# Kernel optimization log

Measured on AMD Instinct MI355X. Metric: run time of the kernel, lower is better.

The kernel has to match this reference:

```python
import jax, jax.numpy as jnp
import numpy as np

B, C, H, W = 4, 256, 64, 64
C8 = C // 8


def setup_inputs() -> dict:
    key = jax.random.key(0)
    ks = jax.random.split(key, 8)
    s = 1.0 / np.sqrt(C)
    return {
        "x_ccd": jax.random.normal(ks[0], (B, C, H, W), jnp.float32),
        "x_dem": jax.random.normal(ks[1], (B, C, H, W), jnp.float32),
        "Wq": jax.random.normal(ks[2], (C8, C), jnp.float32) * s,
        "bq": jax.random.normal(ks[3], (C8,), jnp.float32) * 0.01,
        "Wk": jax.random.normal(ks[4], (C8, C), jnp.float32) * s,
        "bk": jax.random.normal(ks[5], (C8,), jnp.float32) * 0.01,
        "Wv": jax.random.normal(ks[6], (C, C), jnp.float32) * s,
        "bv": jax.random.normal(ks[7], (C,), jnp.float32) * 0.01,
        "gamma": jnp.zeros((1,), jnp.float32),
    }


def reference(x_ccd, x_dem, Wq, bq, Wk, bk, Wv, bv, gamma):
    b, c, h, w = x_ccd.shape
    n = h * w
    xc = x_ccd.reshape(b, c, n)  # [B,C,N]
    xd = x_dem.reshape(b, c, n)
    # 1x1 convs == per-pixel linear projections
    q = jnp.einsum("oc,bcn->bno", Wq, xc) + bq  # [B,N,C8]
    k = jnp.einsum("oc,bcn->bon", Wk, xd) + bk[None, :, None]  # [B,C8,N]
    energy = jnp.einsum("bno,bom->bnm", q, k)  # [B,N,N]
    attention = jax.nn.softmax(energy, axis=-1)
    v = jnp.einsum("oc,bcn->bon", Wv, xd) + bv[None, :, None]  # [B,C,N]
    out = jnp.einsum("bom,bnm->bon", v, attention)  # value @ attention^T
    out = out.reshape(b, c, h, w)
    return gamma * out + x_ccd
```

## Files before the change

kernel.cpp:

```cpp
#include <hip/hip_runtime.h>

typedef unsigned short u16;
typedef unsigned int u32;
typedef short v8s __attribute__((ext_vector_type(8)));
typedef float v16f __attribute__((ext_vector_type(16)));

#define MFMA(a, b, c) __builtin_amdgcn_mfma_f32_32x32x16_bf16(a, b, c, 0, 0, 0)
#define L2E 1.44269504088896f

union U8 { v8s s; uint4 u4; u32 u[4]; };

__device__ __forceinline__ u16 f2bf(float x) {
    u32 u = __float_as_uint(x);
    return (u16)((u + 0x7FFFu + ((u >> 16) & 1u)) >> 16);
}
__device__ __forceinline__ u32 pk2(float a, float b) {
    return (u32)f2bf(a) | ((u32)f2bf(b) << 16);
}
__device__ __forceinline__ u32 pkz(float e0, float e1) {
    return __builtin_amdgcn_perm(__float_as_uint(e1), __float_as_uint(e0), 0x07060302u);
}


__global__ __launch_bounds__(256) void prep_w_kernel(
    const float* __restrict__ Wq, const float* __restrict__ bq,
    const float* __restrict__ Wk, const float* __restrict__ bk,
    const float* __restrict__ Wv, const float* __restrict__ bv,
    u16* __restrict__ WfT, float* __restrict__ ball)
{
    int tid = blockIdx.x * 256 + threadIdx.x;
    if (tid < 81920) {
        int ch = tid >> 8, c = tid & 255;
        float w;
        if (ch < 32)      w = Wq[ch * 256 + c];
        else if (ch < 64) w = Wk[(ch - 32) * 256 + c] * L2E;
        else              w = Wv[(ch - 64) * 256 + c];
        int tile = (ch >> 5) * 16 + (c >> 4);
        int lane = ((c >> 3) & 1) * 32 + (ch & 31);
        WfT[tile * 512 + lane * 8 + (c & 7)] = f2bf(w);
    } else if (tid < 82240) {
        int i = tid - 81920;
        float bb;
        if (i < 32)      bb = bq[i];
        else if (i < 64) bb = bk[i - 32] * L2E;
        else             bb = bv[i - 64];
        ball[i] = bb;
    }
}

__global__ __launch_bounds__(256, 2) void proj_kernel(
    const float* __restrict__ xc, const float* __restrict__ xd,
    const u16* __restrict__ WfT, const float* __restrict__ ball,
    u16* __restrict__ qfT, u16* __restrict__ kfT, u16* __restrict__ vfT)
{
    __shared__ u16 xls[2][32][264];
    int blk = blockIdx.x, b = blk >> 7, n0 = (blk & 127) * 32;
    int t = threadIdx.x, lane = t & 63, wv = t >> 6;
    int hl = lane >> 5, l31 = lane & 31;

#pragma unroll
    for (int p = 0; p < 4; p++) {
        int s = p * 256 + t;
        int arr = s >> 9, c4 = (s >> 3) & 63, n4s = s & 7;
        const float* src = arr ? xd : xc;
        size_t g0 = ((size_t)(b * 256 + c4 * 4)) * 4096 + n0 + n4s * 4;
        float4 r0 = *(const float4*)&src[g0];
        float4 r1 = *(const float4*)&src[g0 + 4096];
        float4 r2 = *(const float4*)&src[g0 + 8192];
        float4 r3 = *(const float4*)&src[g0 + 12288];
        *(uint2*)&xls[arr][n4s * 4 + 0][c4 * 4] = make_uint2(pk2(r0.x, r1.x), pk2(r2.x, r3.x));
        *(uint2*)&xls[arr][n4s * 4 + 1][c4 * 4] = make_uint2(pk2(r0.y, r1.y), pk2(r2.y, r3.y));
        *(uint2*)&xls[arr][n4s * 4 + 2][c4 * 4] = make_uint2(pk2(r0.z, r1.z), pk2(r2.z, r3.z));
        *(uint2*)&xls[arr][n4s * 4 + 3][c4 * 4] = make_uint2(pk2(r0.w, r1.w), pk2(r2.w, r3.w));
    }
    __syncthreads();

    int jobs[3];
    int nj;
    if (wv == 0)      { jobs[0] = 0; jobs[1] = 2; jobs[2] = 0; nj = 2; }
    else if (wv == 1) { jobs[0] = 1; jobs[1] = 3; jobs[2] = 0; nj = 2; }
    else if (wv == 2) { jobs[0] = 4; jobs[1] = 5; jobs[2] = 6; nj = 3; }
    else              { jobs[0] = 7; jobs[1] = 8; jobs[2] = 9; nj = 3; }

    int nt = blk & 127;
    int n = n0 + l31;
    int vl = ((n >> 3) & 1) * 32, tk = n >> 4, j8 = n & 7;

    for (int jj = 0; jj < nj; jj++) {
        int j = jobs[jj];
        int arr = (j != 0);
        const u16* wb = WfT + (size_t)(j * 16) * 512 + lane * 8;
        v16f acc = {};
#pragma unroll
        for (int kc = 0; kc < 16; kc++) {
            U8 bx, a;
            bx.u4 = *(const uint4*)&xls[arr][l31][kc * 16 + hl * 8];
            a.u4  = *(const uint4*)(wb + (size_t)kc * 512);
            acc = MFMA(a.s, bx.s, acc);
        }
        if (j <= 1) {
            u16* dst = j ? kfT : qfT;
#pragma unroll
            for (int i = 0; i < 8; i++) {
                int r = 2 * i;
                int row = (r & 3) + 8 * (r >> 2) + 4 * hl;
                float b0 = ball[j * 32 + row], b1 = ball[j * 32 + row + 1];
                u32 st = pk2(acc[r] + b0, acc[r + 1] + b1);
                size_t off = (((size_t)(b * 128 + nt) * 2 + (row >> 4)) * 512)
                           + (((row >> 3) & 1) * 32 + l31) * 8 + (row & 7);
                *(u32*)&dst[off] = st;
            }
        } else {
            int vi = j - 2;
            u16* vdst = vfT + (((size_t)(b * 8 + vi) * 256 + tk) * 512) + vl * 8 + j8;
#pragma unroll
            for (int r = 0; r < 16; r++) {
                int row = (r & 3) + 8 * (r >> 2) + 4 * hl;
                vdst[row * 8] = f2bf(acc[r] + ball[64 + vi * 32 + row]);
            }
        }
    }
}

__global__ __launch_bounds__(512, 2) void flash_kernel(
    const u16* __restrict__ qfT, const u16* __restrict__ kfT,
    const u16* __restrict__ vfT, const float* __restrict__ xccd,
    const float* __restrict__ gptr, float* __restrict__ outp)
{
    __shared__ float red[2][2][4][16][64];
    __shared__ float lred[2][32];

    const int t = threadIdx.x, lane = t & 63, wv = t >> 6;
    const int hl = lane >> 5, l31 = lane & 31;
    const int blk = blockIdx.x;
    const int b = (blk & 7) >> 1;
    const int qt = ((blk >> 3) << 1) | (blk & 1);
    const int kh = wv & 1, chh = (wv >> 1) & 1, qh = wv >> 2;
    const int n0 = qt * 64 + qh * 32;
    const int chbase = chh * 128;

    U8 qf0, qf1;
    {
        const u16* qp = qfT + ((size_t)(b * 128 + (n0 >> 5)) * 2) * 512 + lane * 8;
        qf0.u4 = *(const uint4*)qp;
        qf1.u4 = *(const uint4*)(qp + 512);
    }
    U8 ones;
#pragma unroll
    for (int i = 0; i < 8; i++) ones.s[i] = (short)0x3F80;

    v16f acc[4] = {};
    v16f lac = {};

    const u16* kbase = kfT + ((size_t)b * 128 * 2) * 512 + lane * 8;
    const u16* vbase = vfT + ((size_t)(b * 8 + chh * 4) * 256) * 512 + lane * 8;

    U8 kA[2], kB[2], vA[4][2], vB[4][2];

    auto load_frags = [&](int it, U8 (&kf)[2], U8 (&vf)[4][2]) {
        const int kt = it * 2 + kh;
        kf[0].u4 = *(const uint4*)(kbase + (size_t)(kt * 2) * 512);
        kf[1].u4 = *(const uint4*)(kbase + (size_t)(kt * 2 + 1) * 512);
        const int tk = it * 4 + kh * 2;
#pragma unroll
        for (int ct = 0; ct < 4; ct++) {
            const u16* vp = vbase + ((size_t)(ct * 256 + tk)) * 512;
            vf[ct][0].u4 = *(const uint4*)vp;
            vf[ct][1].u4 = *(const uint4*)(vp + 512);
        }
    };

    load_frags(0, kA, vA);

    auto step = [&](int it, U8 (&kf)[2], U8 (&vf)[4][2], U8 (&kn)[2], U8 (&vn)[4][2]) {
        if (it < 63) load_frags(it + 1, kn, vn);
        v16f E = {};
        E = MFMA(kf[0].s, qf0.s, E);
        E = MFMA(kf[1].s, qf1.s, E);
        u32 pkv[8];
#pragma unroll
        for (int j = 0; j < 8; j++)
            pkv[j] = pkz(exp2f(E[2 * j]), exp2f(E[2 * j + 1]));
#pragma unroll
        for (int kc = 0; kc < 2; kc++) {
            const int pb = kc * 4;
            u32 p01 = pkv[pb], p23 = pkv[pb + 1];
            u32 p45 = pkv[pb + 2], p67 = pkv[pb + 3];
            u32 s0 = hl ? p01 : p45;
            u32 s1 = hl ? p23 : p67;
            u32 r0 = (u32)__shfl_xor((int)s0, 32, 64);
            u32 r1 = (u32)__shfl_xor((int)s1, 32, 64);
            U8 B;
            B.u[0] = hl ? r0 : p01;
            B.u[1] = hl ? r1 : p23;
            B.u[2] = hl ? p45 : r0;
            B.u[3] = hl ? p67 : r1;
            lac = MFMA(ones.s, B.s, lac);
#pragma unroll
            for (int ct = 0; ct < 4; ct++)
                acc[ct] = MFMA(vf[ct][kc].s, B.s, acc[ct]);
        }
    };
#pragma unroll 1
    for (int it = 0; it < 64; it += 2) {
        step(it, kA, vA, kB, vB);
        step(it + 1, kB, vB, kA, vA);
    }
    if (kh == 1) {
#pragma unroll
        for (int ct = 0; ct < 4; ct++)
#pragma unroll
            for (int r = 0; r < 16; r++)
                red[qh][chh][ct][r][lane] = acc[ct][r];
        if (chh == 0 && lane < 32) lred[qh][l31] = lac[0];
    }
    __syncthreads();
    if (kh == 0) {
        const float g = gptr[0];
        const float sc = g / (lac[0] + lred[qh][l31]);
#pragma unroll
        for (int ct = 0; ct < 4; ct++)
#pragma unroll
            for (int r = 0; r < 16; r++) {
                float v = acc[ct][r] + red[qh][chh][ct][r][lane];
                int ch = chbase + ct * 32 + (r & 3) + 8 * (r >> 2) + 4 * hl;
                size_t ga = ((size_t)(b * 256 + ch)) * 4096 + n0 + l31;
                outp[ga] = v * sc + xccd[ga];
            }
    }
}

extern "C" void kernel_launch(void* const* d_in, const int* in_sizes, int n_in,
                              void* d_out, int out_size, void* d_ws, size_t ws_size,
                              hipStream_t stream)
{
    const float* xc    = (const float*)d_in[0];
    const float* xd    = (const float*)d_in[1];
    const float* Wq    = (const float*)d_in[2];
    const float* bq    = (const float*)d_in[3];
    const float* Wk    = (const float*)d_in[4];
    const float* bk    = (const float*)d_in[5];
    const float* Wv    = (const float*)d_in[6];
    const float* bv    = (const float*)d_in[7];
    const float* gamma = (const float*)d_in[8];
    float* out = (float*)d_out;

    u16* qfT  = (u16*)d_ws;
    u16* kfT  = qfT + (size_t)524288;
    u16* vfT  = kfT + (size_t)524288;
    u16* WfT  = vfT + (size_t)4194304;
    float* bl = (float*)(WfT + 81920);

    prep_w_kernel<<<322, 256, 0, stream>>>(Wq, bq, Wk, bk, Wv, bv, WfT, bl);
    proj_kernel<<<512, 256, 0, stream>>>(xc, xd, WfT, bl, qfT, kfT, vfT);
    flash_kernel<<<256, 512, 0, stream>>>(qfT, kfT, vfT, xc, gamma, out);
}
```

Baseline: 173.6 us.

## Split flash attention key range four ways with 32-query tiles per block

Each block now handles 32 queries instead of 64 and splits the key dimension across four waves per channel half instead of two. This doubles the grid to 512 blocks and raises the launch bound to 4 blocks per CU, aiming for better occupancy and CU coverage. The cost is a two-stage shared-memory reduction of the partial accumulators with an extra barrier, and each block redundantly streams K/V for fewer queries, which raises total K/V traffic.

New measurement: 601.7 us. 3.47x slower.

```diff
diff --git a/kernel.cpp b/kernel.cpp
--- a/kernel.cpp
+++ b/kernel.cpp
@@ -122,26 +122,26 @@
     }
 }
 
-__global__ __launch_bounds__(512, 2) void flash_kernel(
+__global__ __launch_bounds__(512, 4) void flash_kernel(
     const u16* __restrict__ qfT, const u16* __restrict__ kfT,
     const u16* __restrict__ vfT, const float* __restrict__ xccd,
     const float* __restrict__ gptr, float* __restrict__ outp)
 {
     __shared__ float red[2][2][4][16][64];
-    __shared__ float lred[2][32];
+    __shared__ float lred[4][32];
 
     const int t = threadIdx.x, lane = t & 63, wv = t >> 6;
     const int hl = lane >> 5, l31 = lane & 31;
     const int blk = blockIdx.x;
     const int b = (blk & 7) >> 1;
     const int qt = ((blk >> 3) << 1) | (blk & 1);
-    const int kh = wv & 1, chh = (wv >> 1) & 1, qh = wv >> 2;
-    const int n0 = qt * 64 + qh * 32;
+    const int n0 = qt * 32;
+    const int kh = wv & 3, chh = wv >> 2;
     const int chbase = chh * 128;
 
     U8 qf0, qf1;
     {
-        const u16* qp = qfT + ((size_t)(b * 128 + (n0 >> 5)) * 2) * 512 + lane * 8;
+        const u16* qp = qfT + ((size_t)(b * 128 + qt) * 2) * 512 + lane * 8;
         qf0.u4 = *(const uint4*)qp;
         qf1.u4 = *(const uint4*)(qp + 512);
     }
@@ -157,11 +157,11 @@
 
     U8 kA[2], kB[2], vA[4][2], vB[4][2];
 
-    auto load_frags = [&](int it, U8 (&kf)[2], U8 (&vf)[4][2]) {
-        const int kt = it * 2 + kh;
+    auto load_frags = [&](int i, U8 (&kf)[2], U8 (&vf)[4][2]) {
+        const int kt = i * 4 + kh;
         kf[0].u4 = *(const uint4*)(kbase + (size_t)(kt * 2) * 512);
         kf[1].u4 = *(const uint4*)(kbase + (size_t)(kt * 2 + 1) * 512);
-        const int tk = it * 4 + kh * 2;
+        const int tk = kt * 2;
 #pragma unroll
         for (int ct = 0; ct < 4; ct++) {
             const u16* vp = vbase + ((size_t)(ct * 256 + tk)) * 512;
@@ -173,7 +173,7 @@
     load_frags(0, kA, vA);
 
     auto step = [&](int it, U8 (&kf)[2], U8 (&vf)[4][2], U8 (&kn)[2], U8 (&vn)[4][2]) {
-        if (it < 63) load_frags(it + 1, kn, vn);
+        if (it + 1 < 32) load_frags(it + 1, kn, vn);
         v16f E = {};
         E = MFMA(kf[0].s, qf0.s, E);
         E = MFMA(kf[1].s, qf1.s, E);
@@ -195,34 +195,51 @@
             B.u[1] = hl ? r1 : p23;
             B.u[2] = hl ? p45 : r0;
             B.u[3] = hl ? p67 : r1;
-            lac = MFMA(ones.s, B.s, lac);
+            if (chh == 0) lac = MFMA(ones.s, B.s, lac);
 #pragma unroll
             for (int ct = 0; ct < 4; ct++)
                 acc[ct] = MFMA(vf[ct][kc].s, B.s, acc[ct]);
         }
     };
 #pragma unroll 1
-    for (int it = 0; it < 64; it += 2) {
+    for (int it = 0; it < 32; it += 2) {
         step(it, kA, vA, kB, vB);
         step(it + 1, kB, vB, kA, vA);
     }
-    if (kh == 1) {
+    if (chh == 0 && lane < 32) lred[kh][l31] = lac[0];
+    if (kh == 1 || kh == 3) {
+        const int slot = kh >> 1;
 #pragma unroll
         for (int ct = 0; ct < 4; ct++)
 #pragma unroll
             for (int r = 0; r < 16; r++)
-                red[qh][chh][ct][r][lane] = acc[ct][r];
-        if (chh == 0 && lane < 32) lred[qh][l31] = lac[0];
+                red[chh][slot][ct][r][lane] = acc[ct][r];
+    }
+    __syncthreads();
+    if (kh == 0 || kh == 2) {
+        const int slot = kh >> 1;
+#pragma unroll
+        for (int ct = 0; ct < 4; ct++)
+#pragma unroll
+            for (int r = 0; r < 16; r++)
+                acc[ct][r] += red[chh][slot][ct][r][lane];
+        if (kh == 2) {
+#pragma unroll
+            for (int ct = 0; ct < 4; ct++)
+#pragma unroll
+                for (int r = 0; r < 16; r++)
+                    red[chh][1][ct][r][lane] = acc[ct][r];
+        }
     }
     __syncthreads();
     if (kh == 0) {
         const float g = gptr[0];
-        const float sc = g / (lac[0] + lred[qh][l31]);
+        const float sc = g / (lred[0][l31] + lred[1][l31] + lred[2][l31] + lred[3][l31]);
 #pragma unroll
         for (int ct = 0; ct < 4; ct++)
 #pragma unroll
             for (int r = 0; r < 16; r++) {
-                float v = acc[ct][r] + red[qh][chh][ct][r][lane];
+                float v = acc[ct][r] + red[chh][1][ct][r][lane];
                 int ch = chbase + ct * 32 + (r & 3) + 8 * (r >> 2) + 4 * hl;
                 size_t ga = ((size_t)(b * 256 + ch)) * 4096 + n0 + l31;
                 outp[ga] = v * sc + xccd[ga];
@@ -253,5 +270,5 @@
 
     prep_w_kernel<<<322, 256, 0, stream>>>(Wq, bq, Wk, bk, Wv, bv, WfT, bl);
     proj_kernel<<<512, 256, 0, stream>>>(xc, xd, WfT, bl, qfT, kfT, vfT);
-    flash_kernel<<<256, 512, 0, stream>>>(qfT, kfT, vfT, xc, gamma, out);
-}
+    flash_kernel<<<512, 512, 0, stream>>>(qfT, kfT, vfT, xc, gamma, out);
+}
```
